# Kernel optimization log

Measured on AMD Instinct MI355X. Metric: run time of the kernel, lower is better.

## Reference

```python
import jax, jax.numpy as jnp
import numpy as np

N = 50000      # num nodes
E = 800000     # num edges (avg degree 16)
D = 128        # in_dim


def setup_inputs() -> dict:
    key = jax.random.key(0)
    k1, k2, k3, k4, k5, k6 = jax.random.split(key, 6)
    h = jax.random.normal(k1, (N, D), dtype=jnp.float32)
    deg = jax.random.uniform(k2, (N,), dtype=jnp.float32)  # degree-norm scalars d
    # xavier_normal_ with gain=1.414 on Linear(2D, 1)
    std = 1.414 * np.sqrt(2.0 / (2 * D + 1))
    gate_w = jax.random.normal(k3, (1, 2 * D), dtype=jnp.float32) * std
    gate_b = jax.random.normal(k4, (1,), dtype=jnp.float32) * 0.01
    src = jax.random.randint(k5, (E,), 0, N, dtype=jnp.int64)
    dst = jax.random.randint(k6, (E,), 0, N, dtype=jnp.int64)
    return {"h": h, "deg": deg, "gate_w": gate_w, "gate_b": gate_b,
            "src": src, "dst": dst}


def reference(h, deg, gate_w, gate_b, src, dst):
    # Split gate weight so we never materialize the [E, 2D] concat:
    # gate(cat([h_dst, h_src])) == h_dst @ w_d.T + h_src @ w_s.T + b
    d_feat = h.shape[1]
    w_d = gate_w[:, :d_feat]   # [1, D] applied to dst features
    w_s = gate_w[:, d_feat:]   # [1, D] applied to src features
    hs = h[src]                # [E, D] gather of source node features
    hd = h[dst]                # [E, D] gather of dest node features
    a = jnp.tanh(hd @ w_d.T + hs @ w_s.T + gate_b).squeeze(-1)  # [E]
    e = a * deg[dst] * deg[src]                                  # [E] (dropout = identity, eval)
    # message = h[src] * e ; aggregate sum at dst
    z = jax.ops.segment_sum(hs * e[:, None], dst, num_segments=h.shape[0])  # [N, D]
    return z
```

## Files before the change

kernel.cpp:

```cpp
#include <hip/hip_runtime.h>

#define N_NODES 50000
#define N_EDGES 800000
#define DFEAT   128
#define CAP     48
#define NBINS   256
#define NPB     196
#define BINCAP  3700
#define CHUNK   4096

__device__ __forceinline__ unsigned bf16_rne(float f) {
    unsigned u = __float_as_uint(f);
    return (u + 0x7FFFu + ((u >> 16) & 1u)) >> 16;
}

__global__ __launch_bounds__(256) void k1_dots(const float* __restrict__ h,
                                               const float* __restrict__ gate_w,
                                               const float* __restrict__ deg,
                                               float4* __restrict__ nodetab,
                                               int* __restrict__ counts,
                                               unsigned* __restrict__ hb,
                                               int* __restrict__ gbin) {
    if (gbin && blockIdx.x == 0) {
        for (int i = threadIdx.x; i < NBINS; i += 256) gbin[i] = 0;
    }
    int node = (blockIdx.x * 256 + threadIdx.x) >> 6;
    int lane = threadIdx.x & 63;
    if (node >= N_NODES) return;
    const float2* h2 = (const float2*)(h + (size_t)node * DFEAT);
    float2 hv = h2[lane];
    if (hb) {
        unsigned lo = bf16_rne(hv.x);
        unsigned hi = bf16_rne(hv.y);
        hb[(size_t)node * 64 + lane] = lo | (hi << 16);
    }
    float2 wd = ((const float2*)gate_w)[lane];
    float2 ws = ((const float2*)(gate_w + DFEAT))[lane];
    float vd = hv.x * wd.x + hv.y * wd.y;
    float vs = hv.x * ws.x + hv.y * ws.y;
    #pragma unroll
    for (int off = 32; off > 0; off >>= 1) {
        vd += __shfl_down(vd, off, 64);
        vs += __shfl_down(vs, off, 64);
    }
    if (lane == 0) {
        nodetab[node] = make_float4(vd, vs, deg[node], 0.0f);
        counts[node] = 0;
    }
}

__global__ __launch_bounds__(256) void k2a_bin(const int* __restrict__ src,
                                               const int* __restrict__ dst,
                                               const float4* __restrict__ nodetab,
                                               const float* __restrict__ gate_b,
                                               int* __restrict__ gbin_cnt,
                                               uint2* __restrict__ binned) {
    __shared__ uint2 stage[CHUNK];
    __shared__ int bcnt[NBINS], bcur[NBINS], gbase[NBINS];
    int tid = threadIdx.x;
    for (int i = tid; i < NBINS; i += 256) { bcnt[i] = 0; bcur[i] = 0; }
    __syncthreads();

    int e0 = blockIdx.x * CHUNK;
    float bb = gate_b[0];
    for (int i = tid; i < CHUNK; i += 256) {
        int e = e0 + i;
        unsigned m = 0xFFFFFFFFu; float w = 0.f;
        if (e < N_EDGES) {
            int s = src[e], d = dst[e];
            float4 ns = nodetab[s];
            float4 nd = nodetab[d];
            float a = tanhf(nd.x + ns.y + bb);
            w = a * nd.z * ns.z;
            int bin  = d / NPB;
            int dlow = d - bin * NPB;
            m = (unsigned)s | ((unsigned)dlow << 16) | ((unsigned)bin << 24);
            atomicAdd(&bcnt[bin], 1);
        }
        stage[i] = make_uint2(m, __float_as_uint(w));
    }
    __syncthreads();
    for (int i = tid; i < NBINS; i += 256)
        if (bcnt[i] > 0) gbase[i] = atomicAdd(&gbin_cnt[i], bcnt[i]);
    __syncthreads();
    for (int i = tid; i < CHUNK; i += 256) {
        uint2 r = stage[i];
        if (r.x != 0xFFFFFFFFu) {
            int bin = r.x >> 24;
            int pos = atomicAdd(&bcur[bin], 1);
            int idx = gbase[bin] + pos;
            if (idx < BINCAP)
                binned[(size_t)bin * BINCAP + idx] = r;
        }
    }
}

__global__ __launch_bounds__(256) void k2b_bucket(const uint2* __restrict__ binned,
                                                  const int* __restrict__ gbin_cnt,
                                                  unsigned* __restrict__ bucket,
                                                  int* __restrict__ counts) {
    __shared__ int lcnt[NPB];
    __shared__ unsigned lbuck[NPB * CAP];
    int tid = threadIdx.x, bin = blockIdx.x;
    for (int i = tid; i < NPB; i += 256) lcnt[i] = 0;
    __syncthreads();

    int cnt = gbin_cnt[bin]; if (cnt > BINCAP) cnt = BINCAP;
    const uint2* bsrc = binned + (size_t)bin * BINCAP;
    for (int i = tid; i < cnt; i += 256) {
        uint2 r = bsrc[i];
        int dlow = (r.x >> 16) & 0xFF;
        unsigned packed = (r.x & 0xFFFFu) | (bf16_rne(__uint_as_float(r.y)) << 16);
        int pos = atomicAdd(&lcnt[dlow], 1);
        if (pos < CAP) lbuck[dlow * CAP + pos] = packed;
    }
    __syncthreads();

    int nbase = bin * NPB;
    int nvalid = N_NODES - nbase; if (nvalid > NPB) nvalid = NPB;
    for (int i = tid; i < nvalid; i += 256) {
        int c = lcnt[i];
        counts[nbase + i] = (c > CAP) ? CAP : c;
    }
    int limit = nvalid * CAP;
    unsigned* dstp = bucket + (size_t)nbase * CAP;
    for (int i = tid; i < limit; i += 256) dstp[i] = lbuck[i];
}

__global__ __launch_bounds__(256) void k2_edge(const int* __restrict__ src,
                                               const int* __restrict__ dst,
                                               const float4* __restrict__ nodetab,
                                               const float* __restrict__ gate_b,
                                               int* __restrict__ counts,
                                               unsigned* __restrict__ bucket) {
    int e = blockIdx.x * 256 + threadIdx.x;
    if (e >= N_EDGES) return;
    int s = src[e], d = dst[e];
    float4 ns = nodetab[s];
    float4 nd = nodetab[d];
    float a = tanhf(nd.x + ns.y + gate_b[0]);
    float w = a * nd.z * ns.z;
    int pos = atomicAdd(&counts[d], 1);
    if (pos < CAP)
        bucket[(size_t)d * CAP + pos] = (unsigned)s | (bf16_rne(w) << 16);
}

__device__ __forceinline__ void bf4_fma(float4& a, float w, uint2 q) {
    a.x += w * __uint_as_float(q.x << 16);
    a.y += w * __uint_as_float(q.x & 0xFFFF0000u);
    a.z += w * __uint_as_float(q.y << 16);
    a.w += w * __uint_as_float(q.y & 0xFFFF0000u);
}

__global__ __launch_bounds__(256) void k5_gather_bf16(const unsigned* __restrict__ bucket,
                                                      const int* __restrict__ counts,
                                                      const unsigned* __restrict__ hb,
                                                      float* __restrict__ z) {
    int node = (blockIdx.x * 256 + threadIdx.x) >> 6;
    int lane = threadIdx.x & 63;
    if (node >= N_NODES) return;
    int half = lane >> 5;
    int fl   = lane & 31;
    int cnt = counts[node];
    if (cnt > CAP) cnt = CAP;
    const unsigned* b = bucket + (size_t)node * CAP;
    const uint2* hb2 = (const uint2*)hb;

    float4 a0 = make_float4(0.f,0.f,0.f,0.f);
    float4 a1 = make_float4(0.f,0.f,0.f,0.f);
    float4 a2 = make_float4(0.f,0.f,0.f,0.f);
    float4 a3 = make_float4(0.f,0.f,0.f,0.f);

    int last = cnt - 1;
    for (int p = 0; p < cnt; p += 16) {
        int base = p + half;
        int i0 = base;      if (i0 > last) i0 = last;
        int i1 = base + 2;  if (i1 > last) i1 = last;
        int i2 = base + 4;  if (i2 > last) i2 = last;
        int i3 = base + 6;  if (i3 > last) i3 = last;
        int i4 = base + 8;  if (i4 > last) i4 = last;
        int i5 = base + 10; if (i5 > last) i5 = last;
        int i6 = base + 12; if (i6 > last) i6 = last;
        int i7 = base + 14; if (i7 > last) i7 = last;
        unsigned e0 = b[i0], e1 = b[i1], e2 = b[i2], e3 = b[i3];
        unsigned e4 = b[i4], e5 = b[i5], e6 = b[i6], e7 = b[i7];
        uint2 q0 = hb2[(size_t)(e0 & 0xFFFFu) * 32 + fl];
        uint2 q1 = hb2[(size_t)(e1 & 0xFFFFu) * 32 + fl];
        uint2 q2 = hb2[(size_t)(e2 & 0xFFFFu) * 32 + fl];
        uint2 q3 = hb2[(size_t)(e3 & 0xFFFFu) * 32 + fl];
        uint2 q4 = hb2[(size_t)(e4 & 0xFFFFu) * 32 + fl];
        uint2 q5 = hb2[(size_t)(e5 & 0xFFFFu) * 32 + fl];
        uint2 q6 = hb2[(size_t)(e6 & 0xFFFFu) * 32 + fl];
        uint2 q7 = hb2[(size_t)(e7 & 0xFFFFu) * 32 + fl];
        float w0 = (base      <= last) ? __uint_as_float(e0 & 0xFFFF0000u) : 0.f;
        float w1 = (base + 2  <= last) ? __uint_as_float(e1 & 0xFFFF0000u) : 0.f;
        float w2 = (base + 4  <= last) ? __uint_as_float(e2 & 0xFFFF0000u) : 0.f;
        float w3 = (base + 6  <= last) ? __uint_as_float(e3 & 0xFFFF0000u) : 0.f;
        float w4 = (base + 8  <= last) ? __uint_as_float(e4 & 0xFFFF0000u) : 0.f;
        float w5 = (base + 10 <= last) ? __uint_as_float(e5 & 0xFFFF0000u) : 0.f;
        float w6 = (base + 12 <= last) ? __uint_as_float(e6 & 0xFFFF0000u) : 0.f;
        float w7 = (base + 14 <= last) ? __uint_as_float(e7 & 0xFFFF0000u) : 0.f;
        bf4_fma(a0, w0, q0);
        bf4_fma(a1, w1, q1);
        bf4_fma(a2, w2, q2);
        bf4_fma(a3, w3, q3);
        bf4_fma(a0, w4, q4);
        bf4_fma(a1, w5, q5);
        bf4_fma(a2, w6, q6);
        bf4_fma(a3, w7, q7);
    }

    a0.x += a1.x + a2.x + a3.x;
    a0.y += a1.y + a2.y + a3.y;
    a0.z += a1.z + a2.z + a3.z;
    a0.w += a1.w + a2.w + a3.w;

    float ox = __shfl_down(a0.x, 32, 64);
    float oy = __shfl_down(a0.y, 32, 64);
    float oz = __shfl_down(a0.z, 32, 64);
    float ow = __shfl_down(a0.w, 32, 64);
    if (half == 0) {
        a0.x += ox; a0.y += oy; a0.z += oz; a0.w += ow;
        ((float4*)z)[(size_t)node * 32 + fl] = a0;
    }
}

__global__ __launch_bounds__(256) void k5_gather_f32(const unsigned* __restrict__ bucket,
                                                     const int* __restrict__ counts,
                                                     const float* __restrict__ h,
                                                     float* __restrict__ z) {
    int node = (blockIdx.x * 256 + threadIdx.x) >> 6;
    int lane = threadIdx.x & 63;
    if (node >= N_NODES) return;
    int half = lane >> 5;
    int fl   = lane & 31;
    int cnt = counts[node];
    if (cnt > CAP) cnt = CAP;
    const unsigned* b = bucket + (size_t)node * CAP;
    const float4* h4 = (const float4*)h;

    float4 a0 = make_float4(0.f,0.f,0.f,0.f);
    float4 a1 = make_float4(0.f,0.f,0.f,0.f);

    int p = 0;
    for (; p + 4 <= cnt; p += 4) {
        unsigned e0 = b[p     + half];
        unsigned e1 = b[p + 2 + half];
        float4 h0 = h4[(size_t)(e0 & 0xFFFFu) * 32 + fl];
        float4 h1 = h4[(size_t)(e1 & 0xFFFFu) * 32 + fl];
        float w0 = __uint_as_float(e0 & 0xFFFF0000u);
        float w1 = __uint_as_float(e1 & 0xFFFF0000u);
        a0.x += w0*h0.x; a0.y += w0*h0.y; a0.z += w0*h0.z; a0.w += w0*h0.w;
        a1.x += w1*h1.x; a1.y += w1*h1.y; a1.z += w1*h1.z; a1.w += w1*h1.w;
    }
    for (; p < cnt; p += 2) {
        int q = p + half;
        if (q < cnt) {
            unsigned e = b[q];
            float4 hv = h4[(size_t)(e & 0xFFFFu) * 32 + fl];
            float w = __uint_as_float(e & 0xFFFF0000u);
            a0.x += w*hv.x; a0.y += w*hv.y; a0.z += w*hv.z; a0.w += w*hv.w;
        }
    }
    a0.x += a1.x; a0.y += a1.y; a0.z += a1.z; a0.w += a1.w;

    float ox = __shfl_down(a0.x, 32, 64);
    float oy = __shfl_down(a0.y, 32, 64);
    float oz = __shfl_down(a0.z, 32, 64);
    float ow = __shfl_down(a0.w, 32, 64);
    if (half == 0) {
        a0.x += ox; a0.y += oy; a0.z += oz; a0.w += ow;
        ((float4*)z)[(size_t)node * 32 + fl] = a0;
    }
}

extern "C" void kernel_launch(void* const* d_in, const int* in_sizes, int n_in,
                              void* d_out, int out_size, void* d_ws, size_t ws_size,
                              hipStream_t stream) {
    const float* h      = (const float*)d_in[0];
    const float* deg    = (const float*)d_in[1];
    const float* gate_w = (const float*)d_in[2];
    const float* gate_b = (const float*)d_in[3];
    const int*   src    = (const int*)d_in[4];
    const int*   dst    = (const int*)d_in[5];
    float* z = (float*)d_out;

    float4*   nodetab = (float4*)d_ws;
    int*      counts  = (int*)(nodetab + N_NODES);
    unsigned* bucket  = (unsigned*)(counts + N_NODES);
    unsigned* hb      = (unsigned*)(bucket + (size_t)N_NODES * CAP);
    int*      gbin    = (int*)(hb + (size_t)N_NODES * 64);
    uint2*    binned  = (uint2*)(gbin + NBINS);
    const size_t NEED_BF16 = 800000u + 200000u + 9600000u + 12800000u;
    const size_t NEED_BIN  = NEED_BF16 + 1024u + (size_t)NBINS * BINCAP * 8u;
    bool use_bf16 = (ws_size >= NEED_BF16);
    bool use_bin  = (ws_size >= NEED_BIN);

    int nodeBlocks = (N_NODES * 64 + 255) / 256;
    int edgeBlocks = (N_EDGES + 255) / 256;
    int binBlocks  = (N_EDGES + CHUNK - 1) / CHUNK;

    k1_dots<<<nodeBlocks, 256, 0, stream>>>(h, gate_w, deg, nodetab, counts,
                                            use_bf16 ? hb : nullptr,
                                            use_bin ? gbin : nullptr);
    if (use_bin) {
        k2a_bin<<<binBlocks, 256, 0, stream>>>(src, dst, nodetab, gate_b, gbin, binned);
        k2b_bucket<<<NBINS, 256, 0, stream>>>(binned, gbin, bucket, counts);
    } else {
        k2_edge<<<edgeBlocks, 256, 0, stream>>>(src, dst, nodetab, gate_b,
                                                counts, bucket);
    }
    if (use_bf16)
        k5_gather_bf16<<<nodeBlocks, 256, 0, stream>>>(bucket, counts, hb, z);
    else
        k5_gather_f32<<<nodeBlocks, 256, 0, stream>>>(bucket, counts, h, z);
}
```

Baseline: 157.8 us.

## Slice bf16 feature table into 8 column slices for cache-local gather

```diff
diff --git a/kernel.cpp b/kernel.cpp
--- a/kernel.cpp
+++ b/kernel.cpp
@@ -8,6 +8,7 @@
 #define NPB     196
 #define BINCAP  3700
 #define CHUNK   4096
+#define HBS     (N_NODES * 8)
 
 __device__ __forceinline__ unsigned bf16_rne(float f) {
     unsigned u = __float_as_uint(f);
@@ -32,7 +33,8 @@
     if (hb) {
         unsigned lo = bf16_rne(hv.x);
         unsigned hi = bf16_rne(hv.y);
-        hb[(size_t)node * 64 + lane] = lo | (hi << 16);
+        int slice = lane >> 3, u = lane & 7;
+        hb[(size_t)slice * HBS + node * 8 + u] = lo | (hi << 16);
     }
     float2 wd = ((const float2*)gate_w)[lane];
     float2 ws = ((const float2*)(gate_w + DFEAT))[lane];
@@ -145,83 +147,40 @@
         bucket[(size_t)d * CAP + pos] = (unsigned)s | (bf16_rne(w) << 16);
 }
 
-__device__ __forceinline__ void bf4_fma(float4& a, float w, uint2 q) {
-    a.x += w * __uint_as_float(q.x << 16);
-    a.y += w * __uint_as_float(q.x & 0xFFFF0000u);
-    a.z += w * __uint_as_float(q.y << 16);
-    a.w += w * __uint_as_float(q.y & 0xFFFF0000u);
-}
-
-__global__ __launch_bounds__(256) void k5_gather_bf16(const unsigned* __restrict__ bucket,
-                                                      const int* __restrict__ counts,
-                                                      const unsigned* __restrict__ hb,
-                                                      float* __restrict__ z) {
-    int node = (blockIdx.x * 256 + threadIdx.x) >> 6;
-    int lane = threadIdx.x & 63;
-    if (node >= N_NODES) return;
-    int half = lane >> 5;
-    int fl   = lane & 31;
-    int cnt = counts[node];
-    if (cnt > CAP) cnt = CAP;
-    const unsigned* b = bucket + (size_t)node * CAP;
-    const uint2* hb2 = (const uint2*)hb;
-
-    float4 a0 = make_float4(0.f,0.f,0.f,0.f);
-    float4 a1 = make_float4(0.f,0.f,0.f,0.f);
-    float4 a2 = make_float4(0.f,0.f,0.f,0.f);
-    float4 a3 = make_float4(0.f,0.f,0.f,0.f);
-
-    int last = cnt - 1;
-    for (int p = 0; p < cnt; p += 16) {
-        int base = p + half;
-        int i0 = base;      if (i0 > last) i0 = last;
-        int i1 = base + 2;  if (i1 > last) i1 = last;
-        int i2 = base + 4;  if (i2 > last) i2 = last;
-        int i3 = base + 6;  if (i3 > last) i3 = last;
-        int i4 = base + 8;  if (i4 > last) i4 = last;
-        int i5 = base + 10; if (i5 > last) i5 = last;
-        int i6 = base + 12; if (i6 > last) i6 = last;
-        int i7 = base + 14; if (i7 > last) i7 = last;
-        unsigned e0 = b[i0], e1 = b[i1], e2 = b[i2], e3 = b[i3];
-        unsigned e4 = b[i4], e5 = b[i5], e6 = b[i6], e7 = b[i7];
-        uint2 q0 = hb2[(size_t)(e0 & 0xFFFFu) * 32 + fl];
-        uint2 q1 = hb2[(size_t)(e1 & 0xFFFFu) * 32 + fl];
-        uint2 q2 = hb2[(size_t)(e2 & 0xFFFFu) * 32 + fl];
-        uint2 q3 = hb2[(size_t)(e3 & 0xFFFFu) * 32 + fl];
-        uint2 q4 = hb2[(size_t)(e4 & 0xFFFFu) * 32 + fl];
-        uint2 q5 = hb2[(size_t)(e5 & 0xFFFFu) * 32 + fl];
-        uint2 q6 = hb2[(size_t)(e6 & 0xFFFFu) * 32 + fl];
-        uint2 q7 = hb2[(size_t)(e7 & 0xFFFFu) * 32 + fl];
-        float w0 = (base      <= last) ? __uint_as_float(e0 & 0xFFFF0000u) : 0.f;
-        float w1 = (base + 2  <= last) ? __uint_as_float(e1 & 0xFFFF0000u) : 0.f;
-        float w2 = (base + 4  <= last) ? __uint_as_float(e2 & 0xFFFF0000u) : 0.f;
-        float w3 = (base + 6  <= last) ? __uint_as_float(e3 & 0xFFFF0000u) : 0.f;
-        float w4 = (base + 8  <= last) ? __uint_as_float(e4 & 0xFFFF0000u) : 0.f;
-        float w5 = (base + 10 <= last) ? __uint_as_float(e5 & 0xFFFF0000u) : 0.f;
-        float w6 = (base + 12 <= last) ? __uint_as_float(e6 & 0xFFFF0000u) : 0.f;
-        float w7 = (base + 14 <= last) ? __uint_as_float(e7 & 0xFFFF0000u) : 0.f;
-        bf4_fma(a0, w0, q0);
-        bf4_fma(a1, w1, q1);
-        bf4_fma(a2, w2, q2);
-        bf4_fma(a3, w3, q3);
-        bf4_fma(a0, w4, q4);
-        bf4_fma(a1, w5, q5);
-        bf4_fma(a2, w6, q6);
-        bf4_fma(a3, w7, q7);
-    }
-
-    a0.x += a1.x + a2.x + a3.x;
-    a0.y += a1.y + a2.y + a3.y;
-    a0.z += a1.z + a2.z + a3.z;
-    a0.w += a1.w + a2.w + a3.w;
-
-    float ox = __shfl_down(a0.x, 32, 64);
-    float oy = __shfl_down(a0.y, 32, 64);
-    float oz = __shfl_down(a0.z, 32, 64);
-    float ow = __shfl_down(a0.w, 32, 64);
-    if (half == 0) {
-        a0.x += ox; a0.y += oy; a0.z += oz; a0.w += ow;
-        ((float4*)z)[(size_t)node * 32 + fl] = a0;
+__global__ __launch_bounds__(256) void k5_gather_sliced(const unsigned* __restrict__ bucket,
+                                                        const int* __restrict__ counts,
+                                                        const unsigned* __restrict__ hb,
+                                                        float* __restrict__ z) {
+    int slice = blockIdx.x & 7;
+    int nblk  = blockIdx.x >> 3;
+    int wave  = threadIdx.x >> 6;
+    int lane  = threadIdx.x & 63;
+    int eg    = lane >> 3;
+    int u     = lane & 7;
+    const unsigned* hbs = hb + (size_t)slice * HBS;
+
+    #pragma unroll
+    for (int i = 0; i < 4; ++i) {
+        int node = nblk * 16 + wave * 4 + i;
+        int cnt = counts[node];
+        if (cnt > CAP) cnt = CAP;
+        const unsigned* b = bucket + (size_t)node * CAP;
+        float ax = 0.f, ay = 0.f;
+        int last = cnt - 1;
+        for (int p = 0; p < cnt; p += 8) {
+            int idx = p + eg;
+            int ic = (idx > last) ? last : idx;
+            unsigned e = b[ic];
+            unsigned q = hbs[(size_t)(e & 0xFFFFu) * 8 + u];
+            float w = (idx <= last) ? __uint_as_float(e & 0xFFFF0000u) : 0.f;
+            ax += w * __uint_as_float(q << 16);
+            ay += w * __uint_as_float(q & 0xFFFF0000u);
+        }
+        ax += __shfl_down(ax, 32, 64); ay += __shfl_down(ay, 32, 64);
+        ax += __shfl_down(ax, 16, 64); ay += __shfl_down(ay, 16, 64);
+        ax += __shfl_down(ax, 8, 64);  ay += __shfl_down(ay, 8, 64);
+        if (lane < 8)
+            ((float2*)z)[(size_t)node * 64 + slice * 8 + u] = make_float2(ax, ay);
     }
 }
 
@@ -289,29 +248,27 @@
     int*      counts  = (int*)(nodetab + N_NODES);
     unsigned* bucket  = (unsigned*)(counts + N_NODES);
     unsigned* hb      = (unsigned*)(bucket + (size_t)N_NODES * CAP);
-    int*      gbin    = (int*)(hb + (size_t)N_NODES * 64);
+    int*      gbin    = (int*)(hb + (size_t)8 * HBS);
     uint2*    binned  = (uint2*)(gbin + NBINS);
-    const size_t NEED_BF16 = 800000u + 200000u + 9600000u + 12800000u;
-    const size_t NEED_BIN  = NEED_BF16 + 1024u + (size_t)NBINS * BINCAP * 8u;
-    bool use_bf16 = (ws_size >= NEED_BF16);
-    bool use_bin  = (ws_size >= NEED_BIN);
+    const size_t NEED = 800000u + 200000u + 9600000u + 12800000u + 1024u
+                      + (size_t)NBINS * BINCAP * 8u;
+    bool full = (ws_size >= NEED);
 
     int nodeBlocks = (N_NODES * 64 + 255) / 256;
     int edgeBlocks = (N_EDGES + 255) / 256;
     int binBlocks  = (N_EDGES + CHUNK - 1) / CHUNK;
+    int slcBlocks  = (N_NODES / 16) * 8;
 
     k1_dots<<<nodeBlocks, 256, 0, stream>>>(h, gate_w, deg, nodetab, counts,
-                                            use_bf16 ? hb : nullptr,
-                                            use_bin ? gbin : nullptr);
-    if (use_bin) {
+                                            full ? hb : nullptr,
+                                            full ? gbin : nullptr);
+    if (full) {
         k2a_bin<<<binBlocks, 256, 0, stream>>>(src, dst, nodetab, gate_b, gbin, binned);
         k2b_bucket<<<NBINS, 256, 0, stream>>>(binned, gbin, bucket, counts);
+        k5_gather_sliced<<<slcBlocks, 256, 0, stream>>>(bucket, counts, hb, z);
     } else {
         k2_edge<<<edgeBlocks, 256, 0, stream>>>(src, dst, nodetab, gate_b,
                                                 counts, bucket);
-    }
-    if (use_bf16)
-        k5_gather_bf16<<<nodeBlocks, 256, 0, stream>>>(bucket, counts, hb, z);
-    else
-        k5_gather_f32<<<nodeBlocks, 256, 0, stream>>>(bucket, counts, h, z);
-}
+        k5_gather_f32<<<edgeBlocks == 0 ? 1 : nodeBlocks, 256, 0, stream>>>(bucket, counts, h, z);
+    }
+}
```

Result: slower. 208.1 us (+31.9%).
